# Performance work log

Hardware: AMD Instinct MI355X
Metric: run time of the kernel (lower is better)

Reference implementation:

```python
import jax, jax.numpy as jnp
import numpy as np

N_USERS = 200000
N_ITEMS = 100000
N_NODES = N_USERS + N_ITEMS
N_EDGES = 4800000
EMB = 64
BATCH = 4096


def setup_inputs() -> dict:
    key = jax.random.key(0)
    ks = jax.random.split(key, 7)
    user_id = jax.random.randint(ks[0], (BATCH,), 0, N_USERS, dtype=jnp.int64 if jax.config.jax_enable_x64 else jnp.int32)
    item_id = jax.random.randint(ks[1], (BATCH,), 0, N_ITEMS, dtype=jnp.int64 if jax.config.jax_enable_x64 else jnp.int32)
    adj_row = jax.random.randint(ks[2], (N_EDGES,), 0, N_NODES, dtype=jnp.int32)
    adj_col = jax.random.randint(ks[3], (N_EDGES,), 0, N_NODES, dtype=jnp.int32)
    # normalized adjacency values (positive, ~1/deg scale)
    adj_vals = jax.random.uniform(ks[4], (N_EDGES,), dtype=jnp.float32) * 0.1
    user_emb = jax.random.normal(ks[5], (N_USERS, EMB), dtype=jnp.float32)
    item_emb = jax.random.normal(ks[6], (N_ITEMS, EMB), dtype=jnp.float32)
    return {"user_emb": user_emb, "item_emb": item_emb,
            "adj_row": adj_row, "adj_col": adj_col, "adj_vals": adj_vals,
            "user_id": user_id, "item_id": item_id}


def _spmm(row, col, vals, x):
    # sparse [N,N] @ dense [N,D] via gather + segment_sum
    msg = vals[:, None] * x[col]              # [nnz, D]
    return jax.ops.segment_sum(msg, row, num_segments=N_NODES)


def reference(user_emb, item_emb, adj_row, adj_col, adj_vals, user_id, item_id):
    x0 = jnp.concatenate([user_emb, item_emb], axis=0)   # [N, D] ego embeddings
    # single euler step of dx/dt = A@x + e with e = x0, t: 0 -> 1 (dt = 1):
    # z1 = x0 + (A@x0 + x0) = 2*x0 + A@x0
    ax = _spmm(adj_row, adj_col, adj_vals, x0)
    z1 = 2.0 * x0 + ax
    u_all = z1[:N_USERS]
    i_all = z1[N_USERS:]
    return (u_all[user_id], i_all[item_id])
```

## Files before the change

kernel.cpp:

```cpp
#include <hip/hip_runtime.h>

#define N_USERS 200000
#define N_ITEMS 100000
#define N_NODES 300000
#define N_EDGES 4800000
#define EMB 64
#define BATCH 4096
#define NSLOTS (2 * BATCH)
#define NBITMAP ((N_NODES + 31) / 32)
#define CAP 64

typedef unsigned int u32;

__global__ void k_init(int* __restrict__ node2slot, u32* __restrict__ bitmap,
                       u32* __restrict__ slot_count) {
    int i = blockIdx.x * blockDim.x + threadIdx.x;
    if (i < N_NODES) node2slot[i] = -1;
    if (i < NBITMAP) bitmap[i] = 0u;
    if (i < NSLOTS) slot_count[i] = 0u;
}

__global__ void k_map(const int* __restrict__ user_id, const int* __restrict__ item_id,
                      int* __restrict__ node2slot, u32* __restrict__ bitmap) {
    int b = blockIdx.x * blockDim.x + threadIdx.x;
    if (b >= NSLOTS) return;
    int node = (b < BATCH) ? user_id[b] : (N_USERS + item_id[b - BATCH]);
    atomicCAS(&node2slot[node], -1, b);
    atomicOr(&bitmap[node >> 5], 1u << (node & 31));
}

__global__ void k_filter(const int4* __restrict__ adj_row4, const u32* __restrict__ bitmap,
                         const int* __restrict__ node2slot,
                         u32* __restrict__ slot_count, u32* __restrict__ slot_edges) {
    u32 i = blockIdx.x * blockDim.x + threadIdx.x;
    if (i >= N_EDGES / 4) return;
    int4 rr = adj_row4[i];
    u32 e0 = i * 4u;
    #pragma unroll
    for (int k = 0; k < 4; k++) {
        int r = (&rr.x)[k];
        if ((bitmap[r >> 5] >> (r & 31)) & 1u) {
            int s = node2slot[r];
            u32 p = atomicAdd(&slot_count[s], 1u);
            if (p < CAP) slot_edges[(u32)s * CAP + p] = e0 + (u32)k;
        }
    }
}

__global__ void k_accum(const u32* __restrict__ slot_count, const u32* __restrict__ slot_edges,
                        const int* __restrict__ adj_col, const float* __restrict__ vals,
                        const float* __restrict__ user_emb, const float* __restrict__ item_emb,
                        const int* __restrict__ user_id, const int* __restrict__ item_id,
                        float* __restrict__ out) {
    int lane = threadIdx.x & 63;
    u32 s = (u32)(blockIdx.x * blockDim.x + threadIdx.x) >> 6;
    if (s >= NSLOTS) return;
    u32 cnt = slot_count[s];
    if (cnt > CAP) cnt = CAP;
    int c = 0; float v = 0.f;
    if ((u32)lane < cnt) {
        u32 e = slot_edges[s * CAP + (u32)lane];
        c = adj_col[e];
        v = vals[e];
    }
    float a0 = 0.f, a1 = 0.f;
    u32 j = 0;
    for (; j + 2 <= cnt; j += 2) {
        int c0 = __shfl(c, (int)j);     float v0 = __shfl(v, (int)j);
        int c1 = __shfl(c, (int)j + 1); float v1 = __shfl(v, (int)j + 1);
        const float* x0p = (c0 < N_USERS) ? user_emb + (size_t)c0 * EMB
                                          : item_emb + (size_t)(c0 - N_USERS) * EMB;
        const float* x1p = (c1 < N_USERS) ? user_emb + (size_t)c1 * EMB
                                          : item_emb + (size_t)(c1 - N_USERS) * EMB;
        a0 += v0 * x0p[lane];
        a1 += v1 * x1p[lane];
    }
    if (j < cnt) {
        int c0 = __shfl(c, (int)j); float v0 = __shfl(v, (int)j);
        const float* x0p = (c0 < N_USERS) ? user_emb + (size_t)c0 * EMB
                                          : item_emb + (size_t)(c0 - N_USERS) * EMB;
        a0 += v0 * x0p[lane];
    }
    int node = (s < BATCH) ? user_id[s] : (N_USERS + item_id[s - BATCH]);
    const float* xr = (node < N_USERS) ? user_emb + (size_t)node * EMB
                                       : item_emb + (size_t)(node - N_USERS) * EMB;
    out[(size_t)s * EMB + lane] = 2.f * xr[lane] + (a0 + a1);
}

__global__ void k_dup(const int* __restrict__ user_id, const int* __restrict__ item_id,
                      const int* __restrict__ node2slot, float* __restrict__ out) {
    int t = blockIdx.x * blockDim.x + threadIdx.x;
    int o = t >> 6, lane = t & 63;
    if (o >= NSLOTS) return;
    int node = (o < BATCH) ? user_id[o] : (N_USERS + item_id[o - BATCH]);
    int s = node2slot[node];
    if (s != o) out[(size_t)o * EMB + lane] = out[(size_t)s * EMB + lane];
}

extern "C" void kernel_launch(void* const* d_in, const int* in_sizes, int n_in,
                              void* d_out, int out_size, void* d_ws, size_t ws_size,
                              hipStream_t stream) {
    const float* user_emb = (const float*)d_in[0];
    const float* item_emb = (const float*)d_in[1];
    const int* adj_row = (const int*)d_in[2];
    const int* adj_col = (const int*)d_in[3];
    const float* adj_vals = (const float*)d_in[4];
    const int* user_id = (const int*)d_in[5];
    const int* item_id = (const int*)d_in[6];
    float* out = (float*)d_out;

    char* ws = (char*)d_ws;
    size_t off = 0;
    int* node2slot = (int*)(ws + off);  off += ((size_t)N_NODES * 4 + 255) & ~(size_t)255;
    u32* bitmap    = (u32*)(ws + off);  off += ((size_t)NBITMAP * 4 + 255) & ~(size_t)255;
    u32* slot_count= (u32*)(ws + off);  off += ((size_t)NSLOTS * 4 + 255) & ~(size_t)255;
    u32* slot_edges= (u32*)(ws + off);

    const int B = 256;
    k_init<<<(N_NODES + B - 1) / B, B, 0, stream>>>(node2slot, bitmap, slot_count);
    k_map<<<(NSLOTS + B - 1) / B, B, 0, stream>>>(user_id, item_id, node2slot, bitmap);
    k_filter<<<(N_EDGES / 4 + B - 1) / B, B, 0, stream>>>((const int4*)adj_row, bitmap,
                                                          node2slot, slot_count, slot_edges);
    k_accum<<<(NSLOTS * 64 + B - 1) / B, B, 0, stream>>>(slot_count, slot_edges, adj_col,
                                                         adj_vals, user_emb, item_emb,
                                                         user_id, item_id, out);
    k_dup<<<(NSLOTS * 64 + B - 1) / B, B, 0, stream>>>(user_id, item_id, node2slot, out);
}
```

Baseline: 175.0 us.

## Drop node2slot initialization via validated sparse-set lookup and fuse duplicate handling

Removes the kernel that cleared the 300k-entry node2slot table and the bitmap, and instead trusts node2slot entries only after checking that the slot's own batch id maps back to the row. The mapping kernel now writes slots with plain stores and zeroes the slot counters itself. The accumulate kernel resolves each output to its canonical slot directly, so the separate duplicate-copy kernel goes away. In exchange, the edge filter does a random lookup into the larger 1.2MB node2slot array for every edge instead of probing a compact bitmap, which may cost more cache traffic.

```diff
diff --git a/kernel.cpp b/kernel.cpp
--- a/kernel.cpp
+++ b/kernel.cpp
@@ -7,30 +7,22 @@
 #define EMB 64
 #define BATCH 4096
 #define NSLOTS (2 * BATCH)
-#define NBITMAP ((N_NODES + 31) / 32)
 #define CAP 64
 
 typedef unsigned int u32;
 
-__global__ void k_init(int* __restrict__ node2slot, u32* __restrict__ bitmap,
-                       u32* __restrict__ slot_count) {
-    int i = blockIdx.x * blockDim.x + threadIdx.x;
-    if (i < N_NODES) node2slot[i] = -1;
-    if (i < NBITMAP) bitmap[i] = 0u;
-    if (i < NSLOTS) slot_count[i] = 0u;
+__global__ void k_map(const int* __restrict__ user_id, const int* __restrict__ item_id,
+                      int* __restrict__ node2slot, u32* __restrict__ slot_count) {
+    int b = blockIdx.x * blockDim.x + threadIdx.x;
+    if (b >= NSLOTS) return;
+    slot_count[b] = 0u;
+    int node = (b < BATCH) ? user_id[b] : (N_USERS + item_id[b - BATCH]);
+    node2slot[node] = b;
 }
 
-__global__ void k_map(const int* __restrict__ user_id, const int* __restrict__ item_id,
-                      int* __restrict__ node2slot, u32* __restrict__ bitmap) {
-    int b = blockIdx.x * blockDim.x + threadIdx.x;
-    if (b >= NSLOTS) return;
-    int node = (b < BATCH) ? user_id[b] : (N_USERS + item_id[b - BATCH]);
-    atomicCAS(&node2slot[node], -1, b);
-    atomicOr(&bitmap[node >> 5], 1u << (node & 31));
-}
-
-__global__ void k_filter(const int4* __restrict__ adj_row4, const u32* __restrict__ bitmap,
+__global__ void k_filter(const int4* __restrict__ adj_row4,
                          const int* __restrict__ node2slot,
+                         const int* __restrict__ user_id, const int* __restrict__ item_id,
                          u32* __restrict__ slot_count, u32* __restrict__ slot_edges) {
     u32 i = blockIdx.x * blockDim.x + threadIdx.x;
     if (i >= N_EDGES / 4) return;
@@ -39,10 +31,13 @@
     #pragma unroll
     for (int k = 0; k < 4; k++) {
         int r = (&rr.x)[k];
-        if ((bitmap[r >> 5] >> (r & 31)) & 1u) {
-            int s = node2slot[r];
-            u32 p = atomicAdd(&slot_count[s], 1u);
-            if (p < CAP) slot_edges[(u32)s * CAP + p] = e0 + (u32)k;
+        int s = node2slot[r];
+        if ((u32)s < (u32)NSLOTS) {
+            int node_s = (s < BATCH) ? user_id[s] : (N_USERS + item_id[s - BATCH]);
+            if (node_s == r) {
+                u32 p = atomicAdd(&slot_count[s], 1u);
+                if (p < CAP) slot_edges[(u32)s * CAP + p] = e0 + (u32)k;
+            }
         }
     }
 }
@@ -51,15 +46,17 @@
                         const int* __restrict__ adj_col, const float* __restrict__ vals,
                         const float* __restrict__ user_emb, const float* __restrict__ item_emb,
                         const int* __restrict__ user_id, const int* __restrict__ item_id,
-                        float* __restrict__ out) {
+                        const int* __restrict__ node2slot, float* __restrict__ out) {
     int lane = threadIdx.x & 63;
-    u32 s = (u32)(blockIdx.x * blockDim.x + threadIdx.x) >> 6;
-    if (s >= NSLOTS) return;
-    u32 cnt = slot_count[s];
+    u32 o = (u32)(blockIdx.x * blockDim.x + threadIdx.x) >> 6;
+    if (o >= NSLOTS) return;
+    int node = (o < BATCH) ? user_id[o] : (N_USERS + item_id[o - BATCH]);
+    int cs = node2slot[node];
+    u32 cnt = slot_count[cs];
     if (cnt > CAP) cnt = CAP;
     int c = 0; float v = 0.f;
     if ((u32)lane < cnt) {
-        u32 e = slot_edges[s * CAP + (u32)lane];
+        u32 e = slot_edges[(u32)cs * CAP + (u32)lane];
         c = adj_col[e];
         v = vals[e];
     }
@@ -81,20 +78,9 @@
                                           : item_emb + (size_t)(c0 - N_USERS) * EMB;
         a0 += v0 * x0p[lane];
     }
-    int node = (s < BATCH) ? user_id[s] : (N_USERS + item_id[s - BATCH]);
     const float* xr = (node < N_USERS) ? user_emb + (size_t)node * EMB
                                        : item_emb + (size_t)(node - N_USERS) * EMB;
-    out[(size_t)s * EMB + lane] = 2.f * xr[lane] + (a0 + a1);
-}
-
-__global__ void k_dup(const int* __restrict__ user_id, const int* __restrict__ item_id,
-                      const int* __restrict__ node2slot, float* __restrict__ out) {
-    int t = blockIdx.x * blockDim.x + threadIdx.x;
-    int o = t >> 6, lane = t & 63;
-    if (o >= NSLOTS) return;
-    int node = (o < BATCH) ? user_id[o] : (N_USERS + item_id[o - BATCH]);
-    int s = node2slot[node];
-    if (s != o) out[(size_t)o * EMB + lane] = out[(size_t)s * EMB + lane];
+    out[(size_t)o * EMB + lane] = 2.f * xr[lane] + (a0 + a1);
 }
 
 extern "C" void kernel_launch(void* const* d_in, const int* in_sizes, int n_in,
@@ -112,17 +98,15 @@
     char* ws = (char*)d_ws;
     size_t off = 0;
     int* node2slot = (int*)(ws + off);  off += ((size_t)N_NODES * 4 + 255) & ~(size_t)255;
-    u32* bitmap    = (u32*)(ws + off);  off += ((size_t)NBITMAP * 4 + 255) & ~(size_t)255;
     u32* slot_count= (u32*)(ws + off);  off += ((size_t)NSLOTS * 4 + 255) & ~(size_t)255;
     u32* slot_edges= (u32*)(ws + off);
 
     const int B = 256;
-    k_init<<<(N_NODES + B - 1) / B, B, 0, stream>>>(node2slot, bitmap, slot_count);
-    k_map<<<(NSLOTS + B - 1) / B, B, 0, stream>>>(user_id, item_id, node2slot, bitmap);
-    k_filter<<<(N_EDGES / 4 + B - 1) / B, B, 0, stream>>>((const int4*)adj_row, bitmap,
-                                                          node2slot, slot_count, slot_edges);
+    k_map<<<(NSLOTS + B - 1) / B, B, 0, stream>>>(user_id, item_id, node2slot, slot_count);
+    k_filter<<<(N_EDGES / 4 + B - 1) / B, B, 0, stream>>>((const int4*)adj_row, node2slot,
+                                                          user_id, item_id,
+                                                          slot_count, slot_edges);
     k_accum<<<(NSLOTS * 64 + B - 1) / B, B, 0, stream>>>(slot_count, slot_edges, adj_col,
                                                          adj_vals, user_emb, item_emb,
-                                                         user_id, item_id, out);
-    k_dup<<<(NSLOTS * 64 + B - 1) / B, B, 0, stream>>>(user_id, item_id, node2slot, out);
+                                                         user_id, item_id, node2slot, out);
 }
```

Measured after the change: 178.8 us. +2.2%, slower.
